# Optimization experiments

Hardware: AMD Instinct MI355X
Metric: run time of the kernel (lower is better)

The kernel has to match this reference:

```python
import jax, jax.numpy as jnp
import numpy as np

B, CIN, COUT, H, W, K, KH, KW = 32, 256, 256, 56, 56, 4, 3, 3
STRIDE, PAD = (1, 1), [(1, 1), (1, 1)]


def setup_inputs() -> dict:
    key = jax.random.key(0)
    ks = jax.random.split(key, 8)
    s_w = 1.0 / np.sqrt(CIN * KH * KW)
    return {
        "x": jax.random.normal(ks[0], (B, CIN, H, W), jnp.float32),
        "weight": jax.random.normal(ks[1], (K, COUT, CIN, KH, KW), jnp.float32) * s_w,
        "bias": jax.random.normal(ks[2], (K, COUT), jnp.float32) * s_w,
        "fc1_w": jax.random.normal(ks[3], (K, CIN), jnp.float32) / np.sqrt(CIN),
        "fc1_b": jax.random.normal(ks[4], (K,), jnp.float32) * 0.01,
        "fc2_w": jax.random.normal(ks[5], (K, K), jnp.float32) / np.sqrt(K),
        "fc2_b": jax.random.normal(ks[6], (K,), jnp.float32) * 0.01,
    }


def reference(x, weight, bias, fc1_w, fc1_b, fc2_w, fc2_b):
    # Attention2D: global avg pool -> 1x1 conv (dense) -> relu -> 1x1 conv -> softmax
    pooled = x.mean(axis=(2, 3))                                  # [B, CIN]
    a = jax.nn.relu(jnp.einsum('bc,kc->bk', pooled, fc1_w) + fc1_b)
    att = jax.nn.softmax(jnp.einsum('bk,jk->bj', a, fc2_w) + fc2_b, axis=1)  # [B, K]

    # Aggregate per-sample weights/bias over K experts
    agg_w = jnp.einsum('bk,koihw->boihw', att, weight)            # [B, COUT, CIN, KH, KW]
    agg_b = att @ bias                                            # [B, COUT]

    # Per-sample conv == grouped conv with groups=B in the torch original
    def conv_one(xi, wi):
        return jax.lax.conv_general_dilated(
            xi[None], wi, window_strides=STRIDE, padding=PAD,
            dimension_numbers=('NCHW', 'OIHW', 'NCHW'))[0]

    out = jax.vmap(conv_one)(x, agg_w)                            # [B, COUT, H, W]
    return out + agg_b[:, :, None, None]
```

## Files before the change

kernel.cpp:

```cpp
#include <hip/hip_runtime.h>
#include <hip/hip_bf16.h>
#include <stdint.h>

#define BB   32
#define CIN  256
#define COUT 256
#define HH   56
#define WW   56
#define HW   3136
#define KEXP 4
#define HP   58

typedef __attribute__((ext_vector_type(8))) short  short8;
typedef __attribute__((ext_vector_type(4))) float  floatx4;

__device__ __forceinline__ unsigned short f2bf(float f) {
    uint32_t u = __float_as_uint(f);
    u = (u + 0x7fffu + ((u >> 16) & 1u)) >> 16;
    return (unsigned short)u;
}
__device__ __forceinline__ float bf2f(unsigned short s) {
    return __uint_as_float(((uint32_t)s) << 16);
}
__device__ __forceinline__ uint32_t pack2(float a, float b) {
    return (uint32_t)f2bf(a) | ((uint32_t)f2bf(b) << 16);
}

__device__ __forceinline__ void async_copy16(const void* gsrc, void* ldst) {
    __builtin_amdgcn_global_load_lds(
        (const __attribute__((address_space(1))) unsigned int*)gsrc,
        (__attribute__((address_space(3))) unsigned int*)ldst, 16, 0, 0);
}

__global__ __launch_bounds__(256) void transpose_pool_kernel(
    const float* __restrict__ x,
    unsigned short* __restrict__ xt,
    float* __restrict__ partial)
{
    __shared__ unsigned short tile[CIN * 62];
    const int bx  = blockIdx.x;
    const int b   = bx / HH;
    const int h   = bx % HH;
    const int tid = threadIdx.x;

    const float* xb = x + (size_t)b * CIN * HW + h * WW;

    for (int i = tid; i < CIN * 14; i += 256) {
        const int c  = i / 14;
        const int wv = i % 14;
        const float4 v = *(const float4*)(xb + (size_t)c * HW + wv * 4);
        uint32_t* p = (uint32_t*)&tile[c * 62 + wv * 4];
        p[0] = pack2(v.x, v.y);
        p[1] = pack2(v.z, v.w);
    }
    __syncthreads();

    {
        float s = 0.f;
        #pragma unroll 8
        for (int i = 0; i < WW; ++i) s += bf2f(tile[tid * 62 + i]);
        partial[((size_t)b * HH + h) * CIN + tid] = s;
    }

    unsigned short* row = xt + (((size_t)b * HP + (h + 1)) * HP) * CIN;
    for (int j = tid; j < WW * 128; j += 256) {
        const int w  = j >> 7;
        const int c2 = (j & 127) * 2;
        const uint32_t v = (uint32_t)tile[c2 * 62 + w]
                         | ((uint32_t)tile[(c2 + 1) * 62 + w] << 16);
        *(uint32_t*)&row[(w + 1) * CIN + c2] = v;
    }

    if (tid < 128) {
        ((uint32_t*)&row[0])[tid]          = 0u;
        ((uint32_t*)&row[57 * CIN])[tid]   = 0u;
    }
    if (h == 0) {
        uint32_t* r0  = (uint32_t*)(xt + ((size_t)b * HP + 0)  * HP * CIN);
        uint32_t* r57 = (uint32_t*)(xt + ((size_t)b * HP + 57) * HP * CIN);
        for (int i = tid; i < HP * 128; i += 256) { r0[i] = 0u; r57[i] = 0u; }
    }
}

__global__ __launch_bounds__(256) void attn_kernel(
    const float* __restrict__ partial,
    const float* __restrict__ fc1w,
    const float* __restrict__ fc1b,
    const float* __restrict__ fc2w,
    const float* __restrict__ fc2b,
    float* __restrict__ att)
{
    __shared__ float pl[CIN];
    const int b   = blockIdx.x;
    const int tid = threadIdx.x;

    float s = 0.f;
    const float* pp = partial + (size_t)b * HH * CIN + tid;
    #pragma unroll 8
    for (int h = 0; h < HH; ++h) s += pp[h * CIN];
    pl[tid] = s * (1.0f / (float)HW);
    __syncthreads();

    if (tid < 64) {
        const int lane = tid;
        float sk[KEXP] = {0.f, 0.f, 0.f, 0.f};
        #pragma unroll
        for (int c0 = 0; c0 < CIN; c0 += 64) {
            const float p = pl[c0 + lane];
            #pragma unroll
            for (int k = 0; k < KEXP; ++k) sk[k] += p * fc1w[k * CIN + c0 + lane];
        }
        #pragma unroll
        for (int off = 32; off > 0; off >>= 1) {
            #pragma unroll
            for (int k = 0; k < KEXP; ++k) sk[k] += __shfl_down(sk[k], off);
        }
        if (lane == 0) {
            float a[KEXP];
            #pragma unroll
            for (int k = 0; k < KEXP; ++k) a[k] = fmaxf(sk[k] + fc1b[k], 0.f);
            float z[KEXP], m = -1e30f;
            #pragma unroll
            for (int j = 0; j < KEXP; ++j) {
                float t = fc2b[j];
                #pragma unroll
                for (int k = 0; k < KEXP; ++k) t += a[k] * fc2w[j * KEXP + k];
                z[j] = t;
                m = fmaxf(m, t);
            }
            float den = 0.f;
            #pragma unroll
            for (int j = 0; j < KEXP; ++j) { z[j] = expf(z[j] - m); den += z[j]; }
            const float inv = 1.0f / den;
            #pragma unroll
            for (int j = 0; j < KEXP; ++j) att[b * KEXP + j] = z[j] * inv;
        }
    }
}

__global__ __launch_bounds__(256) void aggw_kernel(
    const float* __restrict__ weight,
    const float* __restrict__ bias,
    const float* __restrict__ att,
    unsigned short* __restrict__ aggw,
    float* __restrict__ aggb)
{
    __shared__ float accw[CIN * 9];
    const int bx  = blockIdx.x;
    const int o   = bx >> 2;
    const int b0  = (bx & 3) * 8;
    const int tid = threadIdx.x;

    float wreg[KEXP][9];
    #pragma unroll
    for (int k = 0; k < KEXP; ++k) {
        const float* wk = weight + (size_t)(k * COUT + o) * (CIN * 9);
        #pragma unroll
        for (int j = 0; j < 9; ++j) wreg[k][j] = wk[j * 256 + tid];
    }
    float bvals[KEXP];
    #pragma unroll
    for (int k = 0; k < KEXP; ++k) bvals[k] = bias[k * COUT + o];

    for (int bi = 0; bi < 8; ++bi) {
        const int b = b0 + bi;
        float av[KEXP];
        #pragma unroll
        for (int k = 0; k < KEXP; ++k) av[k] = att[b * KEXP + k];

        __syncthreads();
        #pragma unroll
        for (int j = 0; j < 9; ++j) {
            float r = 0.f;
            #pragma unroll
            for (int k = 0; k < KEXP; ++k) r += av[k] * wreg[k][j];
            accw[j * 256 + tid] = r;
        }
        __syncthreads();

        for (int i = tid; i < 9 * 128; i += 256) {
            const int j  = i >> 7;
            const int cp = (i & 127) * 2;
            const uint32_t v = pack2(accw[cp * 9 + j], accw[(cp + 1) * 9 + j]);
            *(uint32_t*)&aggw[(((size_t)b * 9 + j) * COUT + o) * CIN + cp] = v;
        }
        if (tid == 0) {
            float sb = 0.f;
            #pragma unroll
            for (int k = 0; k < KEXP; ++k) sb += av[k] * bvals[k];
            aggb[b * COUT + o] = sb;
        }
    }
}

#define PHASE(MH, KS, LOADB, STAGE_STMT, VM_STMT) do {                         \
    const char* Ap_ = lds + bufoff + (KS) * 16384 + lnoff;                     \
    const char* Bp_ = lds + bufoff + 32768 + (KS) * 16384 + lnoff;             \
    short8 af_[4];                                                             \
    if (LOADB) {                                                               \
        _Pragma("unroll")                                                      \
        for (int ni_ = 0; ni_ < 4; ++ni_)                                      \
            bf[ni_] = *(const short8*)(Bp_ + wn * 4096 + ni_ * 1024);          \
    }                                                                          \
    _Pragma("unroll")                                                          \
    for (int mi_ = 0; mi_ < 4; ++mi_)                                          \
        af_[mi_] = *(const short8*)(Ap_ + wm * 8192 + (MH) * 4096 + mi_ * 1024); \
    STAGE_STMT;                                                                \
    __builtin_amdgcn_sched_barrier(0);                                         \
    __builtin_amdgcn_s_barrier();                                              \
    asm volatile("s_waitcnt lgkmcnt(0)");                                      \
    __builtin_amdgcn_sched_barrier(0);                                         \
    __builtin_amdgcn_s_setprio(1);                                             \
    _Pragma("unroll")                                                          \
    for (int mi_ = 0; mi_ < 4; ++mi_)                                          \
        _Pragma("unroll")                                                      \
        for (int ni_ = 0; ni_ < 4; ++ni_)                                      \
            acc[(MH) * 4 + mi_][ni_] = __builtin_amdgcn_mfma_f32_16x16x32_bf16( \
                af_[mi_], bf[ni_], acc[(MH) * 4 + mi_][ni_], 0, 0, 0);         \
    __builtin_amdgcn_s_setprio(0);                                             \
    __builtin_amdgcn_sched_barrier(0);                                         \
    VM_STMT;                                                                   \
    __builtin_amdgcn_sched_barrier(0);                                         \
    __builtin_amdgcn_s_barrier();                                              \
    __builtin_amdgcn_sched_barrier(0);                                         \
} while (0)

__global__ __launch_bounds__(512, 2) void conv_gemm_kernel(
    const unsigned short* __restrict__ xt,
    const unsigned short* __restrict__ aggw,
    const float* __restrict__ aggb,
    float* __restrict__ out)
{
    __shared__ __attribute__((aligned(128))) char lds[131072];

    const int bx = blockIdx.x;
    const int wg = (bx & 7) * 52 + (bx >> 3);
    const int b  = wg / 13;
    const int p0 = (wg - b * 13) * 256;

    const int tid  = threadIdx.x;
    const int wave = tid >> 6;
    const int lane = tid & 63;
    const int wm   = wave >> 2;
    const int wn   = wave & 3;
    const int m    = lane & 15;
    const int q    = lane >> 4;
    const int lnoff = m * 64 + ((q ^ (m >> 1)) & 3) * 16;

    const char* aggw_b = (const char*)aggw + (size_t)b * (9 * COUT * CIN * 2);
    const char* xt_b   = (const char*)xt   + (size_t)b * (HP * HP * CIN * 2);

    int aoff0, aoff1, boff0, boff1;
    {
        int n = tid, r = n >> 2, u = n & 3, sw = (u ^ (r >> 1)) & 3;
        aoff0 = r * 512 + sw * 16;
        int p = p0 + r; int pv = (p < HW) ? p : 0;
        int h = pv / WW, w = pv - h * WW;
        boff0 = ((h + 1) * HP + (w + 1)) * 512 + sw * 16;

        n = 512 + tid; r = n >> 2; u = n & 3; sw = (u ^ (r >> 1)) & 3;
        aoff1 = r * 512 + sw * 16;
        p = p0 + r; pv = (p < HW) ? p : 0;
        h = pv / WW; w = pv - h * WW;
        boff1 = ((h + 1) * HP + (w + 1)) * 512 + sw * 16;
    }

    auto stageA = [&](int kt, int ks) {
        const int ga = (kt >> 2) * (COUT * CIN * 2) + (kt & 3) * 128 + ks * 64;
        char* d = lds + (kt & 1) * 65536 + ks * 16384 + wave * 1024;
        async_copy16(aggw_b + (size_t)(ga + aoff0), d);
        async_copy16(aggw_b + (size_t)(ga + aoff1), d + 8192);
    };
    auto stageB = [&](int kt, int ks) {
        const int rs = kt >> 2;
        const int gb = ((rs / 3 - 1) * HP + (rs % 3 - 1)) * 512
                     + (kt & 3) * 128 + ks * 64;
        char* d = lds + (kt & 1) * 65536 + 32768 + ks * 16384 + wave * 1024;
        async_copy16(xt_b + (size_t)(gb + boff0), d);
        async_copy16(xt_b + (size_t)(gb + boff1), d + 8192);
    };

    floatx4 acc[8][4];
    #pragma unroll
    for (int a_ = 0; a_ < 8; ++a_)
        #pragma unroll
        for (int n_ = 0; n_ < 4; ++n_)
            #pragma unroll
            for (int e_ = 0; e_ < 4; ++e_) acc[a_][n_][e_] = 0.f;

    stageA(0, 0); stageB(0, 0);
    stageA(0, 1); stageB(0, 1);
    stageA(1, 0); stageB(1, 0);
    __builtin_amdgcn_sched_barrier(0);
    asm volatile("s_waitcnt vmcnt(4)");
    __builtin_amdgcn_sched_barrier(0);
    __builtin_amdgcn_s_barrier();
    __builtin_amdgcn_sched_barrier(0);

    #pragma unroll 1
    for (int i = 0; i < 18; ++i) {
        const int t0 = 2 * i;
        {
            const int bufoff = 0;
            short8 bf[4];
            PHASE(0, 0, 1, stageA(t0 + 1, 1), ((void)0));
            PHASE(1, 0, 0, stageB(t0 + 1, 1), ((void)0));
            PHASE(1, 1, 1, if (i < 17) stageA(t0 + 2, 0), ((void)0));
            PHASE(0, 1, 0, if (i < 17) stageB(t0 + 2, 0),
                  if (i < 17) { asm volatile("s_waitcnt vmcnt(4)"); }
                  else        { asm volatile("s_waitcnt vmcnt(0)"); });
        }
        {
            const int bufoff = 65536;
            const int t1 = 2 * i + 1;
            short8 bf[4];
            PHASE(0, 0, 1, if (i < 17) stageA(t1 + 1, 1), ((void)0));
            PHASE(1, 0, 0, if (i < 17) stageB(t1 + 1, 1), ((void)0));
            PHASE(1, 1, 1, if (i < 17) stageA(t1 + 2, 0), ((void)0));
            PHASE(0, 1, 0, if (i < 17) stageB(t1 + 2, 0),
                  asm volatile("s_waitcnt vmcnt(4)"));
        }
    }

    float* outb = out + (size_t)b * COUT * HW;
    const int g4 = q * 4;
    #pragma unroll
    for (int am = 0; am < 8; ++am) {
        const int o = wm * 128 + am * 16 + g4;
        #pragma unroll
        for (int e = 0; e < 4; ++e) {
            const float bv = aggb[b * COUT + o + e];
            #pragma unroll
            for (int ni = 0; ni < 4; ++ni) {
                const int p = p0 + wn * 64 + ni * 16 + m;
                if (p < HW) outb[(size_t)(o + e) * HW + p] = acc[am][ni][e] + bv;
            }
        }
    }
}

extern "C" void kernel_launch(void* const* d_in, const int* in_sizes, int n_in,
                              void* d_out, int out_size, void* d_ws, size_t ws_size,
                              hipStream_t stream) {
    const float* x      = (const float*)d_in[0];
    const float* weight = (const float*)d_in[1];
    const float* bias   = (const float*)d_in[2];
    const float* fc1w   = (const float*)d_in[3];
    const float* fc1b   = (const float*)d_in[4];
    const float* fc2w   = (const float*)d_in[5];
    const float* fc2b   = (const float*)d_in[6];
    float* out = (float*)d_out;

    char* ws = (char*)d_ws;
    unsigned short* xt      = (unsigned short*)(ws);
    unsigned short* aggw    = (unsigned short*)(ws + 55115776);
    float*          partial = (float*)(ws + 92864512);
    float*          att     = (float*)(ws + 94699520);
    float*          aggb    = (float*)(ws + 94700032);

    transpose_pool_kernel<<<BB * HH, 256, 0, stream>>>(x, xt, partial);
    attn_kernel<<<BB, 256, 0, stream>>>(partial, fc1w, fc1b, fc2w, fc2b, att);
    aggw_kernel<<<COUT * 4, 256, 0, stream>>>(weight, bias, att, aggw, aggb);
    conv_gemm_kernel<<<BB * 13, 512, 0, stream>>>(xt, aggw, aggb, out);
}
```

Baseline: 364.0 us.

## Restructure conv GEMM main loop into two-barrier tiles with register double-buffered fragments

Replaces the four-phase-per-tile schedule, which had two barriers and an lgkmcnt(0) wait per phase, with a tile macro that preloads A/B fragments into separate registers. LDS reads for the next MFMA group are interleaved with the current group's MFMAs, and each tile now uses only two workgroup barriers. The last iteration is peeled so the i<17 conditionals disappear from the loop. The goal is to cut barrier and LDS-wait stalls between MFMA batches. In exchange it uses more VGPRs for the extra fragment buffers and drops the explicit lgkmcnt waits, so it depends on the compiler's dependency tracking for LDS reads.

New measurement: 353.7 us. 2.8% less time.

```diff
diff --git a/kernel.cpp b/kernel.cpp
--- a/kernel.cpp
+++ b/kernel.cpp
@@ -193,34 +193,50 @@
     }
 }
 
-#define PHASE(MH, KS, LOADB, STAGE_STMT, VM_STMT) do {                         \
-    const char* Ap_ = lds + bufoff + (KS) * 16384 + lnoff;                     \
-    const char* Bp_ = lds + bufoff + 32768 + (KS) * 16384 + lnoff;             \
-    short8 af_[4];                                                             \
-    if (LOADB) {                                                               \
-        _Pragma("unroll")                                                      \
-        for (int ni_ = 0; ni_ < 4; ++ni_)                                      \
-            bf[ni_] = *(const short8*)(Bp_ + wn * 4096 + ni_ * 1024);          \
-    }                                                                          \
-    _Pragma("unroll")                                                          \
-    for (int mi_ = 0; mi_ < 4; ++mi_)                                          \
-        af_[mi_] = *(const short8*)(Ap_ + wm * 8192 + (MH) * 4096 + mi_ * 1024); \
-    STAGE_STMT;                                                                \
-    __builtin_amdgcn_sched_barrier(0);                                         \
-    __builtin_amdgcn_s_barrier();                                              \
-    asm volatile("s_waitcnt lgkmcnt(0)");                                      \
-    __builtin_amdgcn_sched_barrier(0);                                         \
+#define MM(AB, AF, BF) do {                                                    \
     __builtin_amdgcn_s_setprio(1);                                             \
     _Pragma("unroll")                                                          \
     for (int mi_ = 0; mi_ < 4; ++mi_)                                          \
         _Pragma("unroll")                                                      \
         for (int ni_ = 0; ni_ < 4; ++ni_)                                      \
-            acc[(MH) * 4 + mi_][ni_] = __builtin_amdgcn_mfma_f32_16x16x32_bf16( \
-                af_[mi_], bf[ni_], acc[(MH) * 4 + mi_][ni_], 0, 0, 0);         \
+            acc[(AB) + mi_][ni_] = __builtin_amdgcn_mfma_f32_16x16x32_bf16(    \
+                AF[mi_], BF[ni_], acc[(AB) + mi_][ni_], 0, 0, 0);              \
     __builtin_amdgcn_s_setprio(0);                                             \
+} while (0)
+
+#define TILE(BUF, S1A, S1B, S2A, S2B, VMSTMT) do {                             \
+    const char* A0_ = lds + (BUF) + lnoff;                                     \
+    const char* B0_ = lds + (BUF) + 32768 + lnoff;                             \
+    short8 a0[4], a1[4], a2[4], a3[4], b0[4], b1[4];                           \
+    _Pragma("unroll")                                                          \
+    for (int i_ = 0; i_ < 4; ++i_)                                             \
+        a0[i_] = *(const short8*)(A0_ + wm * 8192 + i_ * 1024);                \
+    _Pragma("unroll")                                                          \
+    for (int i_ = 0; i_ < 4; ++i_)                                             \
+        b0[i_] = *(const short8*)(B0_ + wn * 4096 + i_ * 1024);                \
+    _Pragma("unroll")                                                          \
+    for (int i_ = 0; i_ < 4; ++i_)                                             \
+        a1[i_] = *(const short8*)(A0_ + wm * 8192 + 4096 + i_ * 1024);         \
+    S1A; S1B;                                                                  \
+    MM(0, a0, b0);                                                             \
+    _Pragma("unroll")                                                          \
+    for (int i_ = 0; i_ < 4; ++i_)                                             \
+        a2[i_] = *(const short8*)(A0_ + 16384 + wm * 8192 + 4096 + i_ * 1024); \
+    _Pragma("unroll")                                                          \
+    for (int i_ = 0; i_ < 4; ++i_)                                             \
+        b1[i_] = *(const short8*)(B0_ + 16384 + wn * 4096 + i_ * 1024);        \
+    MM(4, a1, b0);                                                             \
     __builtin_amdgcn_sched_barrier(0);                                         \
-    VM_STMT;                                                                   \
+    __builtin_amdgcn_s_barrier();                                              \
     __builtin_amdgcn_sched_barrier(0);                                         \
+    S2A; S2B;                                                                  \
+    _Pragma("unroll")                                                          \
+    for (int i_ = 0; i_ < 4; ++i_)                                             \
+        a3[i_] = *(const short8*)(A0_ + 16384 + wm * 8192 + i_ * 1024);        \
+    MM(4, a2, b1);                                                             \
+    MM(0, a3, b1);                                                             \
+    __builtin_amdgcn_sched_barrier(0);                                         \
+    VMSTMT;                                                                    \
     __builtin_amdgcn_s_barrier();                                              \
     __builtin_amdgcn_sched_barrier(0);                                         \
 } while (0)
@@ -298,29 +314,23 @@
     __builtin_amdgcn_sched_barrier(0);
 
     #pragma unroll 1
-    for (int i = 0; i < 18; ++i) {
+    for (int i = 0; i < 17; ++i) {
         const int t0 = 2 * i;
-        {
-            const int bufoff = 0;
-            short8 bf[4];
-            PHASE(0, 0, 1, stageA(t0 + 1, 1), ((void)0));
-            PHASE(1, 0, 0, stageB(t0 + 1, 1), ((void)0));
-            PHASE(1, 1, 1, if (i < 17) stageA(t0 + 2, 0), ((void)0));
-            PHASE(0, 1, 0, if (i < 17) stageB(t0 + 2, 0),
-                  if (i < 17) { asm volatile("s_waitcnt vmcnt(4)"); }
-                  else        { asm volatile("s_waitcnt vmcnt(0)"); });
-        }
-        {
-            const int bufoff = 65536;
-            const int t1 = 2 * i + 1;
-            short8 bf[4];
-            PHASE(0, 0, 1, if (i < 17) stageA(t1 + 1, 1), ((void)0));
-            PHASE(1, 0, 0, if (i < 17) stageB(t1 + 1, 1), ((void)0));
-            PHASE(1, 1, 1, if (i < 17) stageA(t1 + 2, 0), ((void)0));
-            PHASE(0, 1, 0, if (i < 17) stageB(t1 + 2, 0),
-                  asm volatile("s_waitcnt vmcnt(4)"));
-        }
-    }
+        const int t1 = 2 * i + 1;
+        TILE(0,
+             stageA(t0 + 1, 1), stageB(t0 + 1, 1),
+             stageA(t0 + 2, 0), stageB(t0 + 2, 0),
+             asm volatile("s_waitcnt vmcnt(4)"));
+        TILE(65536,
+             stageA(t1 + 1, 1), stageB(t1 + 1, 1),
+             stageA(t1 + 2, 0), stageB(t1 + 2, 0),
+             asm volatile("s_waitcnt vmcnt(4)"));
+    }
+    TILE(0,
+         stageA(35, 1), stageB(35, 1),
+         ((void)0), ((void)0),
+         asm volatile("s_waitcnt vmcnt(0)"));
+    TILE(65536, ((void)0), ((void)0), ((void)0), ((void)0), ((void)0));
 
     float* outb = out + (size_t)b * COUT * HW;
     const int g4 = q * 4;
```

## Shrink conv GEMM tile to 256x128 with triple-buffered K=32 pipeline

Applied to the files above, without the earlier changes.

The conv GEMM tile changes from 256 out-channels by 256 pixels to 256 by 128, and the launch grows from 416 to 800 workgroups. The K step drops to 32 with three LDS buffers (72KB total), one barrier per step, and launch bounds raised to allow 4 waves per SIMD. The aim is better CU occupancy and load balance, since 416 blocks leaves the device partly idle or in an uneven last wave. The cost is lower data reuse per tile, meaning more global traffic for the weights and activations, and more barriers relative to the MFMA work.

Result: faster. 351.1 us (-3.5%).

```diff
diff --git a/kernel.cpp b/kernel.cpp
--- a/kernel.cpp
+++ b/kernel.cpp
@@ -193,56 +193,54 @@
     }
 }
 
-#define PHASE(MH, KS, LOADB, STAGE_STMT, VM_STMT) do {                         \
-    const char* Ap_ = lds + bufoff + (KS) * 16384 + lnoff;                     \
-    const char* Bp_ = lds + bufoff + 32768 + (KS) * 16384 + lnoff;             \
-    short8 af_[4];                                                             \
-    if (LOADB) {                                                               \
-        _Pragma("unroll")                                                      \
-        for (int ni_ = 0; ni_ < 4; ++ni_)                                      \
-            bf[ni_] = *(const short8*)(Bp_ + wn * 4096 + ni_ * 1024);          \
-    }                                                                          \
+#define TILE_COMPUTE(BUFOFF) do {                                              \
+    const char* A_ = lds + (BUFOFF) + lnoff;                                   \
+    const char* B_ = lds + (BUFOFF) + 16384 + lnoff;                           \
+    short8 af[4], bf[4];                                                       \
+    _Pragma("unroll")                                                          \
+    for (int ni_ = 0; ni_ < 4; ++ni_)                                          \
+        bf[ni_] = *(const short8*)(B_ + wn * 4096 + ni_ * 1024);               \
     _Pragma("unroll")                                                          \
     for (int mi_ = 0; mi_ < 4; ++mi_)                                          \
-        af_[mi_] = *(const short8*)(Ap_ + wm * 8192 + (MH) * 4096 + mi_ * 1024); \
-    STAGE_STMT;                                                                \
-    __builtin_amdgcn_sched_barrier(0);                                         \
-    __builtin_amdgcn_s_barrier();                                              \
-    asm volatile("s_waitcnt lgkmcnt(0)");                                      \
-    __builtin_amdgcn_sched_barrier(0);                                         \
+        af[mi_] = *(const short8*)(A_ + wm * 4096 + mi_ * 1024);               \
     __builtin_amdgcn_s_setprio(1);                                             \
     _Pragma("unroll")                                                          \
     for (int mi_ = 0; mi_ < 4; ++mi_)                                          \
         _Pragma("unroll")                                                      \
         for (int ni_ = 0; ni_ < 4; ++ni_)                                      \
-            acc[(MH) * 4 + mi_][ni_] = __builtin_amdgcn_mfma_f32_16x16x32_bf16( \
-                af_[mi_], bf[ni_], acc[(MH) * 4 + mi_][ni_], 0, 0, 0);         \
+            acc[mi_][ni_] = __builtin_amdgcn_mfma_f32_16x16x32_bf16(           \
+                af[mi_], bf[ni_], acc[mi_][ni_], 0, 0, 0);                     \
     __builtin_amdgcn_s_setprio(0);                                             \
+} while (0)
+
+#define STEP(TBUF, STAGE_STMT, VM_STMT) do {                                   \
+    STAGE_STMT;                                                                \
+    __builtin_amdgcn_sched_barrier(0);                                         \
+    TILE_COMPUTE(TBUF);                                                        \
     __builtin_amdgcn_sched_barrier(0);                                         \
     VM_STMT;                                                                   \
-    __builtin_amdgcn_sched_barrier(0);                                         \
     __builtin_amdgcn_s_barrier();                                              \
     __builtin_amdgcn_sched_barrier(0);                                         \
 } while (0)
 
-__global__ __launch_bounds__(512, 2) void conv_gemm_kernel(
+__global__ __launch_bounds__(512, 4) void conv_gemm_kernel(
     const unsigned short* __restrict__ xt,
     const unsigned short* __restrict__ aggw,
     const float* __restrict__ aggb,
     float* __restrict__ out)
 {
-    __shared__ __attribute__((aligned(128))) char lds[131072];
+    __shared__ __attribute__((aligned(128))) char lds[73728];
 
     const int bx = blockIdx.x;
-    const int wg = (bx & 7) * 52 + (bx >> 3);
-    const int b  = wg / 13;
-    const int p0 = (wg - b * 13) * 256;
+    const int wg = (bx & 7) * 100 + (bx >> 3);
+    const int b  = wg / 25;
+    const int p0 = (wg - b * 25) * 128;
 
     const int tid  = threadIdx.x;
     const int wave = tid >> 6;
     const int lane = tid & 63;
-    const int wm   = wave >> 2;
-    const int wn   = wave & 3;
+    const int wm   = wave >> 1;
+    const int wn   = wave & 1;
     const int m    = lane & 15;
     const int q    = lane >> 4;
     const int lnoff = m * 64 + ((q ^ (m >> 1)) & 3) * 16;
@@ -250,90 +248,69 @@
     const char* aggw_b = (const char*)aggw + (size_t)b * (9 * COUT * CIN * 2);
     const char* xt_b   = (const char*)xt   + (size_t)b * (HP * HP * CIN * 2);
 
-    int aoff0, aoff1, boff0, boff1;
+    int aoff0, aoff1, boff0;
     {
         int n = tid, r = n >> 2, u = n & 3, sw = (u ^ (r >> 1)) & 3;
         aoff0 = r * 512 + sw * 16;
+
+        n = 512 + tid; r = n >> 2; u = n & 3; sw = (u ^ (r >> 1)) & 3;
+        aoff1 = r * 512 + sw * 16;
+
+        n = tid; r = n >> 2; u = n & 3; sw = (u ^ (r >> 1)) & 3;
         int p = p0 + r; int pv = (p < HW) ? p : 0;
         int h = pv / WW, w = pv - h * WW;
         boff0 = ((h + 1) * HP + (w + 1)) * 512 + sw * 16;
-
-        n = 512 + tid; r = n >> 2; u = n & 3; sw = (u ^ (r >> 1)) & 3;
-        aoff1 = r * 512 + sw * 16;
-        p = p0 + r; pv = (p < HW) ? p : 0;
-        h = pv / WW; w = pv - h * WW;
-        boff1 = ((h + 1) * HP + (w + 1)) * 512 + sw * 16;
-    }
-
-    auto stageA = [&](int kt, int ks) {
-        const int ga = (kt >> 2) * (COUT * CIN * 2) + (kt & 3) * 128 + ks * 64;
-        char* d = lds + (kt & 1) * 65536 + ks * 16384 + wave * 1024;
-        async_copy16(aggw_b + (size_t)(ga + aoff0), d);
-        async_copy16(aggw_b + (size_t)(ga + aoff1), d + 8192);
+    }
+
+    auto stage = [&](int kt, char* buf) {
+        const int rs = kt >> 3;
+        const int c2 = (kt & 7) * 64;
+        const int ga = rs * (COUT * CIN * 2) + c2;
+        const int gb = ((rs / 3 - 1) * HP + (rs % 3 - 1)) * 512 + c2;
+        char* dA = buf + wave * 1024;
+        async_copy16(aggw_b + (size_t)(ga + aoff0), dA);
+        async_copy16(aggw_b + (size_t)(ga + aoff1), dA + 8192);
+        async_copy16(xt_b   + (size_t)(gb + boff0), buf + 16384 + wave * 1024);
     };
-    auto stageB = [&](int kt, int ks) {
-        const int rs = kt >> 2;
-        const int gb = ((rs / 3 - 1) * HP + (rs % 3 - 1)) * 512
-                     + (kt & 3) * 128 + ks * 64;
-        char* d = lds + (kt & 1) * 65536 + 32768 + ks * 16384 + wave * 1024;
-        async_copy16(xt_b + (size_t)(gb + boff0), d);
-        async_copy16(xt_b + (size_t)(gb + boff1), d + 8192);
-    };
-
-    floatx4 acc[8][4];
+
+    floatx4 acc[4][4];
     #pragma unroll
-    for (int a_ = 0; a_ < 8; ++a_)
+    for (int a_ = 0; a_ < 4; ++a_)
         #pragma unroll
         for (int n_ = 0; n_ < 4; ++n_)
             #pragma unroll
             for (int e_ = 0; e_ < 4; ++e_) acc[a_][n_][e_] = 0.f;
 
-    stageA(0, 0); stageB(0, 0);
-    stageA(0, 1); stageB(0, 1);
-    stageA(1, 0); stageB(1, 0);
+    stage(0, lds);
+    stage(1, lds + 24576);
     __builtin_amdgcn_sched_barrier(0);
-    asm volatile("s_waitcnt vmcnt(4)");
-    __builtin_amdgcn_sched_barrier(0);
+    asm volatile("s_waitcnt vmcnt(3)");
     __builtin_amdgcn_s_barrier();
     __builtin_amdgcn_sched_barrier(0);
 
     #pragma unroll 1
-    for (int i = 0; i < 18; ++i) {
-        const int t0 = 2 * i;
-        {
-            const int bufoff = 0;
-            short8 bf[4];
-            PHASE(0, 0, 1, stageA(t0 + 1, 1), ((void)0));
-            PHASE(1, 0, 0, stageB(t0 + 1, 1), ((void)0));
-            PHASE(1, 1, 1, if (i < 17) stageA(t0 + 2, 0), ((void)0));
-            PHASE(0, 1, 0, if (i < 17) stageB(t0 + 2, 0),
-                  if (i < 17) { asm volatile("s_waitcnt vmcnt(4)"); }
-                  else        { asm volatile("s_waitcnt vmcnt(0)"); });
-        }
-        {
-            const int bufoff = 65536;
-            const int t1 = 2 * i + 1;
-            short8 bf[4];
-            PHASE(0, 0, 1, if (i < 17) stageA(t1 + 1, 1), ((void)0));
-            PHASE(1, 0, 0, if (i < 17) stageB(t1 + 1, 1), ((void)0));
-            PHASE(1, 1, 1, if (i < 17) stageA(t1 + 2, 0), ((void)0));
-            PHASE(0, 1, 0, if (i < 17) stageB(t1 + 2, 0),
-                  asm volatile("s_waitcnt vmcnt(4)"));
-        }
-    }
+    for (int i = 0; i < 23; ++i) {
+        const int t = 3 * i;
+        STEP(0,     stage(t + 2, lds + 49152), asm volatile("s_waitcnt vmcnt(3)"));
+        STEP(24576, stage(t + 3, lds),         asm volatile("s_waitcnt vmcnt(3)"));
+        STEP(49152, stage(t + 4, lds + 24576), asm volatile("s_waitcnt vmcnt(3)"));
+    }
+    STEP(0,     stage(71, lds + 49152), asm volatile("s_waitcnt vmcnt(3)"));
+    STEP(24576, ((void)0),              asm volatile("s_waitcnt vmcnt(0)"));
+    TILE_COMPUTE(49152);
 
     float* outb = out + (size_t)b * COUT * HW;
     const int g4 = q * 4;
     #pragma unroll
-    for (int am = 0; am < 8; ++am) {
-        const int o = wm * 128 + am * 16 + g4;
+    for (int mi = 0; mi < 4; ++mi) {
+        const int o = wm * 64 + mi * 16 + g4;
         #pragma unroll
         for (int e = 0; e < 4; ++e) {
             const float bv = aggb[b * COUT + o + e];
             #pragma unroll
             for (int ni = 0; ni < 4; ++ni) {
                 const int p = p0 + wn * 64 + ni * 16 + m;
-                if (p < HW) outb[(size_t)(o + e) * HW + p] = acc[am][ni][e] + bv;
+                if (p < HW) outb[(size_t)(o + e) * HW + p] = acc[mi][ni][e] + bv;
             }
         }
     }
@@ -361,5 +338,5 @@
     transpose_pool_kernel<<<BB * HH, 256, 0, stream>>>(x, xt, partial);
     attn_kernel<<<BB, 256, 0, stream>>>(partial, fc1w, fc1b, fc2w, fc2b, att);
     aggw_kernel<<<COUT * 4, 256, 0, stream>>>(weight, bias, att, aggw, aggb);
-    conv_gemm_kernel<<<BB * 13, 512, 0, stream>>>(xt, aggw, aggb, out);
-}
+    conv_gemm_kernel<<<BB * 25, 512, 0, stream>>>(xt, aggw, aggb, out);
+}
```
